# Optimization experiments

Hardware: AMD Instinct MI355X
Metric: run time of the kernel (lower is better)

Reference implementation:

```python
import jax, jax.numpy as jnp
import numpy as np

N = 50000
E = 400000
IN_DIM = 128
OUT_DIM = 512
NUM_MASK = 15000


def _init_linear(key, din, dout):
    s = 1.0 / np.sqrt(din)
    return jax.random.uniform(key, (din, dout), jnp.float32, -s, s)


def setup_inputs() -> dict:
    key = jax.random.key(0)
    ks = jax.random.split(key, 20)
    attr = jax.random.normal(ks[0], (N, IN_DIM), jnp.float32)
    src = jax.random.randint(ks[1], (E,), 0, N, jnp.int32)
    dst = jax.random.randint(ks[2], (E,), 0, N, jnp.int32)
    mask_nodes = jax.random.randint(ks[3], (NUM_MASK,), 0, N, jnp.int32)
    mask_token = jnp.zeros((1, IN_DIM), jnp.float32)
    dims = [(IN_DIM, OUT_DIM), (OUT_DIM, OUT_DIM), (OUT_DIM, OUT_DIM), (OUT_DIM, IN_DIM)]
    params = {}
    for i, (din, dout) in enumerate(dims, start=1):
        params[f"w_self{i}"] = _init_linear(ks[3 * i + 1], din, dout)
        params[f"w_neigh{i}"] = _init_linear(ks[3 * i + 2], din, dout)
        params[f"b{i}"] = jnp.zeros((dout,), jnp.float32)
    return dict(attr=attr, mask_token=mask_token, src=src, dst=dst, mask_nodes=mask_nodes, **params)


def sage_conv(h, src, dst, w_self, w_neigh, b):
    # mean aggregation over in-neighbors (DGL SAGEConv, aggregator_type='mean')
    msg = h[src]                                              # [E, d]
    agg = jax.ops.segment_sum(msg, dst, num_segments=N)       # [N, d]
    deg = jax.ops.segment_sum(jnp.ones((E,), h.dtype), dst, num_segments=N)
    h_neigh = agg / jnp.maximum(deg, 1.0)[:, None]
    return h @ w_self + h_neigh @ w_neigh + b


def reference(attr, mask_token, src, dst, mask_nodes,
              w_self1, w_neigh1, b1, w_self2, w_neigh2, b2,
              w_self3, w_neigh3, b3, w_self4, w_neigh4, b4):
    # mask node features with the mask token
    h = attr.at[mask_nodes].set(mask_token[0])
    h = jax.nn.relu(sage_conv(h, src, dst, w_self1, w_neigh1, b1))
    h = sage_conv(h, src, dst, w_self2, w_neigh2, b2)          # encoded
    h = jax.nn.relu(sage_conv(h, src, dst, w_self3, w_neigh3, b3))
    decoded = sage_conv(h, src, dst, w_self4, w_neigh4, b4)
    x_orig = attr[mask_nodes]
    x_rec = decoded[mask_nodes]
    return jnp.mean((x_rec - x_orig) ** 2)
```

## Files before the change

kernel.cpp:

```cpp
#include <hip/hip_runtime.h>
#include <cstdint>
#include <cstddef>

#define IN_DIM 128
#define HID    512

typedef unsigned int   uint32;
typedef unsigned short u16;
typedef __attribute__((ext_vector_type(8))) short bf16x8;
typedef __attribute__((ext_vector_type(4))) float f32x4;

static inline int imin_h(int a, int b) { return a < b ? a : b; }

__device__ __forceinline__ float bfu2f(uint32 u) { return __uint_as_float(u << 16); }
__device__ __forceinline__ u16 f2bf(float f) {
  uint32 x = __float_as_uint(f);
  x += 0x7fffu + ((x >> 16) & 1u);
  return (u16)(x >> 16);
}
__device__ __forceinline__ uint32 pack2(float a, float b) {
  return (uint32)f2bf(a) | ((uint32)f2bf(b) << 16);
}

#define GLOBAL_AS(p) ((const __attribute__((address_space(1))) void*)(p))
#define LDS_AS(p)    ((__attribute__((address_space(3))) void*)(p))

__global__ void k_zero2(int* __restrict__ a, int na, int* __restrict__ b, int nb) {
  const int total = na + nb;
  for (int i = blockIdx.x * blockDim.x + threadIdx.x; i < total; i += gridDim.x * blockDim.x) {
    if (i < na) a[i] = 0;
    else        b[i - na] = 0;
  }
}

__global__ void k_hist(const int* __restrict__ dst, int* __restrict__ deg, int E) {
  for (int e = blockIdx.x * blockDim.x + threadIdx.x; e < E; e += gridDim.x * blockDim.x)
    atomicAdd(&deg[dst[e]], 1);
}

__global__ __launch_bounds__(256)
void k_scan1(const int* __restrict__ deg, int* __restrict__ bsum, int n) {
  __shared__ int sm[256];
  const int base = blockIdx.x * 2048 + threadIdx.x * 8;
  int s = 0;
  if (base + 8 <= n) {
    const uint4 a = *reinterpret_cast<const uint4*>(deg + base);
    const uint4 b = *reinterpret_cast<const uint4*>(deg + base + 4);
    s = (int)(a.x + a.y + a.z + a.w + b.x + b.y + b.z + b.w);
  } else {
    for (int i = 0; i < 8; ++i) if (base + i < n) s += deg[base + i];
  }
  sm[threadIdx.x] = s;
  __syncthreads();
  for (int off = 128; off > 0; off >>= 1) {
    if (threadIdx.x < off) sm[threadIdx.x] += sm[threadIdx.x + off];
    __syncthreads();
  }
  if (threadIdx.x == 0) bsum[blockIdx.x] = sm[0];
}

__global__ __launch_bounds__(256)
void k_scan2(int* __restrict__ bsum, int nb, int* __restrict__ rowptr, int n) {
  __shared__ int sm[256];
  const int v = (threadIdx.x < nb) ? bsum[threadIdx.x] : 0;
  sm[threadIdx.x] = v;
  __syncthreads();
  for (int off = 1; off < 256; off <<= 1) {
    const int t = (threadIdx.x >= off) ? sm[threadIdx.x - off] : 0;
    __syncthreads();
    sm[threadIdx.x] += t;
    __syncthreads();
  }
  if (threadIdx.x < nb) bsum[threadIdx.x] = sm[threadIdx.x] - v;
  if (threadIdx.x == nb - 1) rowptr[n] = sm[threadIdx.x];
}

__global__ __launch_bounds__(256)
void k_scan3(const int* __restrict__ deg, const int* __restrict__ bsum,
             int* __restrict__ rowptr, int* __restrict__ cursor, int n) {
  __shared__ int sm[256];
  const int base = blockIdx.x * 2048 + threadIdx.x * 8;
  int v[8];
  int s = 0;
#pragma unroll
  for (int i = 0; i < 8; ++i) {
    v[i] = (base + i < n) ? deg[base + i] : 0;
    s += v[i];
  }
  sm[threadIdx.x] = s;
  __syncthreads();
  for (int off = 1; off < 256; off <<= 1) {
    const int t = (threadIdx.x >= off) ? sm[threadIdx.x - off] : 0;
    __syncthreads();
    sm[threadIdx.x] += t;
    __syncthreads();
  }
  int run = bsum[blockIdx.x] + sm[threadIdx.x] - s;
#pragma unroll
  for (int i = 0; i < 8; ++i) {
    if (base + i < n) { rowptr[base + i] = run; cursor[base + i] = run; }
    run += v[i];
  }
}

__global__ void k_fill(const int* __restrict__ src, const int* __restrict__ dst,
                       int* __restrict__ cursor, int* __restrict__ col, int E) {
  for (int e = blockIdx.x * blockDim.x + threadIdx.x; e < E; e += gridDim.x * blockDim.x) {
    const int p = atomicAdd(&cursor[dst[e]], 1);
    col[p] = src[e];
  }
}

__global__ void k_cvt(const float4* __restrict__ in, uint2* __restrict__ out, int n4) {
  for (int i = blockIdx.x * blockDim.x + threadIdx.x; i < n4; i += gridDim.x * blockDim.x) {
    const float4 v = in[i];
    out[i] = make_uint2(pack2(v.x, v.y), pack2(v.z, v.w));
  }
}

__global__ void k_mask(const float4* __restrict__ token, const int* __restrict__ mask,
                       uint2* __restrict__ h0, int NM) {
  const int total = NM * (IN_DIM / 4);
  for (int i = blockIdx.x * blockDim.x + threadIdx.x; i < total; i += gridDim.x * blockDim.x) {
    const int m = i >> 5;
    const int c = i & 31;
    const float4 t = token[c];
    h0[(size_t)mask[m] * (IN_DIM / 4) + c] = make_uint2(pack2(t.x, t.y), pack2(t.z, t.w));
  }
}

struct WtJobs {
  const float* W[8];
  u16* Wt[8];
  int K[8];
  int Nn[8];
  int start[9];
};

__global__ __launch_bounds__(256)
void k_wt_all(WtJobs jobs) {
  const int total = jobs.start[8];
  for (int t = blockIdx.x * blockDim.x + threadIdx.x; t < total; t += gridDim.x * blockDim.x) {
    int s = 0;
#pragma unroll
    for (int i = 0; i < 7; ++i) s += (t >= jobs.start[i + 1]) ? 1 : 0;
    const int loc = t - jobs.start[s];
    const int K = jobs.K[s], Nn = jobs.Nn[s];
    const int n = loc / K, k = loc - n * K;
    const size_t idx = ((size_t)(n >> 4) * (K >> 5) + (k >> 5)) * 512 +
                       ((k >> 3) & 3) * 128 + ((n & 15) << 3) + (k & 7);
    jobs.Wt[s][idx] = f2bf(jobs.W[s][(size_t)k * Nn + n]);
  }
}

template <int D, bool REMAP>
__global__ __launch_bounds__(256)
void k_agg(const u16* __restrict__ h, const int* __restrict__ col,
           const int* __restrict__ rowptr, const int* __restrict__ nodes,
           u16* __restrict__ out, int n) {
  constexpr int V = D / 64;
  const int w = blockIdx.x * (blockDim.x >> 6) + (threadIdx.x >> 6);
  if (w >= n) return;
  const int node = REMAP ? nodes[w] : w;
  const int lane = threadIdx.x & 63;
  const int beg = rowptr[node], end = rowptr[node + 1];
  const size_t loff = (size_t)lane * V;
  float acc[V];
#pragma unroll
  for (int j = 0; j < V; ++j) acc[j] = 0.f;

  if constexpr (V == 8) {
    auto L = [&](int e) {
      return *reinterpret_cast<const uint4*>(h + (size_t)col[e] * D + loff);
    };
    uint4 b0{}, b1{}, b2{}, b3{};
    if (beg + 0 < end) b0 = L(beg + 0);
    if (beg + 1 < end) b1 = L(beg + 1);
    if (beg + 2 < end) b2 = L(beg + 2);
    if (beg + 3 < end) b3 = L(beg + 3);
    for (int e = beg; e < end; e += 4) {
      const uint4 c0 = b0, c1 = b1, c2 = b2, c3 = b3;
      if (e + 4 < end) b0 = L(e + 4);
      if (e + 5 < end) b1 = L(e + 5);
      if (e + 6 < end) b2 = L(e + 6);
      if (e + 7 < end) b3 = L(e + 7);
      acc[0] += bfu2f(c0.x & 0xffffu); acc[1] += bfu2f(c0.x >> 16);
      acc[2] += bfu2f(c0.y & 0xffffu); acc[3] += bfu2f(c0.y >> 16);
      acc[4] += bfu2f(c0.z & 0xffffu); acc[5] += bfu2f(c0.z >> 16);
      acc[6] += bfu2f(c0.w & 0xffffu); acc[7] += bfu2f(c0.w >> 16);
      if (e + 1 < end) {
        acc[0] += bfu2f(c1.x & 0xffffu); acc[1] += bfu2f(c1.x >> 16);
        acc[2] += bfu2f(c1.y & 0xffffu); acc[3] += bfu2f(c1.y >> 16);
        acc[4] += bfu2f(c1.z & 0xffffu); acc[5] += bfu2f(c1.z >> 16);
        acc[6] += bfu2f(c1.w & 0xffffu); acc[7] += bfu2f(c1.w >> 16);
      }
      if (e + 2 < end) {
        acc[0] += bfu2f(c2.x & 0xffffu); acc[1] += bfu2f(c2.x >> 16);
        acc[2] += bfu2f(c2.y & 0xffffu); acc[3] += bfu2f(c2.y >> 16);
        acc[4] += bfu2f(c2.z & 0xffffu); acc[5] += bfu2f(c2.z >> 16);
        acc[6] += bfu2f(c2.w & 0xffffu); acc[7] += bfu2f(c2.w >> 16);
      }
      if (e + 3 < end) {
        acc[0] += bfu2f(c3.x & 0xffffu); acc[1] += bfu2f(c3.x >> 16);
        acc[2] += bfu2f(c3.y & 0xffffu); acc[3] += bfu2f(c3.y >> 16);
        acc[4] += bfu2f(c3.z & 0xffffu); acc[5] += bfu2f(c3.z >> 16);
        acc[6] += bfu2f(c3.w & 0xffffu); acc[7] += bfu2f(c3.w >> 16);
      }
    }
  } else {
    auto L = [&](int e) {
      return *reinterpret_cast<const uint32*>(h + (size_t)col[e] * D + loff);
    };
    uint32 b0 = 0, b1 = 0, b2 = 0, b3 = 0;
    if (beg + 0 < end) b0 = L(beg + 0);
    if (beg + 1 < end) b1 = L(beg + 1);
    if (beg + 2 < end) b2 = L(beg + 2);
    if (beg + 3 < end) b3 = L(beg + 3);
    for (int e = beg; e < end; e += 4) {
      const uint32 c0 = b0, c1 = b1, c2 = b2, c3 = b3;
      if (e + 4 < end) b0 = L(e + 4);
      if (e + 5 < end) b1 = L(e + 5);
      if (e + 6 < end) b2 = L(e + 6);
      if (e + 7 < end) b3 = L(e + 7);
      acc[0] += bfu2f(c0 & 0xffffu); acc[1] += bfu2f(c0 >> 16);
      if (e + 1 < end) { acc[0] += bfu2f(c1 & 0xffffu); acc[1] += bfu2f(c1 >> 16); }
      if (e + 2 < end) { acc[0] += bfu2f(c2 & 0xffffu); acc[1] += bfu2f(c2 >> 16); }
      if (e + 3 < end) { acc[0] += bfu2f(c3 & 0xffffu); acc[1] += bfu2f(c3 >> 16); }
    }
  }

  const float inv = 1.0f / fmaxf((float)(end - beg), 1.0f);
  u16* o = out + (size_t)w * D + loff;
  if constexpr (V == 8) {
    uint4 u;
    u.x = pack2(acc[0] * inv, acc[1] * inv);
    u.y = pack2(acc[2] * inv, acc[3] * inv);
    u.z = pack2(acc[4] * inv, acc[5] * inv);
    u.w = pack2(acc[6] * inv, acc[7] * inv);
    *reinterpret_cast<uint4*>(o) = u;
  } else {
    *reinterpret_cast<uint32*>(o) = pack2(acc[0] * inv, acc[1] * inv);
  }
}

template <int DIN, bool RELU>
__global__ __launch_bounds__(512, 4)
void k_gemm_big(const u16* __restrict__ A1, const u16* __restrict__ A2,
                const u16* __restrict__ Wt1, const u16* __restrict__ Wt2,
                const float* __restrict__ bias, u16* __restrict__ out, int M) {
  constexpr int DOUT = HID;
  __shared__ char lds[73728];
  constexpr int KS = DIN / 32;
  constexpr int S  = 2 * KS;
  const int tid = threadIdx.x;
  const int w = tid >> 6, l = tid & 63;
  const int l15 = l & 15, l4 = l >> 4;
  const int wm = w >> 2, wn = w & 3;

  const int nwg  = gridDim.x * gridDim.y;
  const int orig = blockIdx.x + gridDim.x * blockIdx.y;
  const int q = nwg >> 3, r = nwg & 7;
  const int xcd = orig & 7, seq = orig >> 3;
  const int wg = (xcd < r ? xcd * (q + 1) : r * (q + 1) + (xcd - r) * q) + seq;
  const int mt = wg >> 1, nt = wg & 1;
  const int m0 = mt * 128, n0 = nt * 256;

  f32x4 acc[4][4];
#pragma unroll
  for (int i = 0; i < 4; ++i)
#pragma unroll
    for (int j = 0; j < 4; ++j) acc[i][j] = (f32x4){0.f, 0.f, 0.f, 0.f};

  const int arow = min(m0 + w * 16 + l15, M - 1);
  const int kl = l4 * 8;
  const u16* pA1 = A1 + (size_t)arow * DIN + kl;
  const u16* pA2 = A2 + (size_t)arow * DIN + kl;
  const u16* bb1 = Wt1 + ((size_t)(n0 >> 4) + 2 * w) * KS * 512 + (size_t)l * 8;
  const u16* bb2 = Wt2 + ((size_t)(n0 >> 4) + 2 * w) * KS * 512 + (size_t)l * 8;

  auto stage = [&](int s) {
    const int ph = s / KS;
    const int kf = s - ph * KS;
    char* buf = lds + (s % 3) * 24576;
    const u16* a0 = (ph ? pA2 : pA1) + kf * 32;
    const u16* b0 = (ph ? bb2 : bb1) + kf * 512;
    const u16* b1 = b0 + KS * 512;
    __builtin_amdgcn_global_load_lds(GLOBAL_AS(a0), LDS_AS(buf + w * 1024), 16, 0, 0);
    __builtin_amdgcn_global_load_lds(GLOBAL_AS(b0), LDS_AS(buf + 8192 + (2 * w + 0) * 1024), 16, 0, 0);
    __builtin_amdgcn_global_load_lds(GLOBAL_AS(b1), LDS_AS(buf + 8192 + (2 * w + 1) * 1024), 16, 0, 0);
  };

  stage(0);
  stage(1);

#pragma unroll
  for (int s = 0; s < S; ++s) {
    if (s + 1 < S) asm volatile("s_waitcnt vmcnt(3)" ::: "memory");
    else           asm volatile("s_waitcnt vmcnt(0)" ::: "memory");
    __builtin_amdgcn_s_barrier();
    if (s + 2 < S) stage(s + 2);
    char* buf = lds + (s % 3) * 24576;
    bf16x8 af[4], bfr[4];
#pragma unroll
    for (int i = 0; i < 4; ++i)
      af[i] = *reinterpret_cast<const bf16x8*>(buf + (wm * 4 + i) * 1024 + l * 16);
#pragma unroll
    for (int j = 0; j < 4; ++j)
      bfr[j] = *reinterpret_cast<const bf16x8*>(buf + 8192 + (wn * 4 + j) * 1024 + l * 16);
#pragma unroll
    for (int i = 0; i < 4; ++i)
#pragma unroll
      for (int j = 0; j < 4; ++j)
        acc[i][j] = __builtin_amdgcn_mfma_f32_16x16x32_bf16(af[i], bfr[j], acc[i][j], 0, 0, 0);
    asm volatile("s_waitcnt lgkmcnt(0)" ::: "memory");
  }
  __builtin_amdgcn_s_barrier();

  u16* eb = (u16*)(lds + w * 9216);
  float bv[4];
#pragma unroll
  for (int j = 0; j < 4; ++j) bv[j] = bias[n0 + wn * 64 + j * 16 + l15];
#pragma unroll
  for (int i = 0; i < 4; ++i)
#pragma unroll
    for (int j = 0; j < 4; ++j)
#pragma unroll
      for (int r = 0; r < 4; ++r) {
        const int lr = i * 16 + l4 * 4 + r;
        float t = acc[i][j][r] + bv[j];
        if (RELU) t = fmaxf(t, 0.f);
        eb[lr * 72 + j * 16 + l15] = f2bf(t);
      }
  asm volatile("s_waitcnt lgkmcnt(0)" ::: "memory");
#pragma unroll
  for (int p = 0; p < 8; ++p) {
    const int lr = p * 8 + (l >> 3);
    const int row = m0 + wm * 64 + lr;
    if (row < M) {
      const uint4 v = *reinterpret_cast<const uint4*>(eb + lr * 72 + (l & 7) * 8);
      *reinterpret_cast<uint4*>(out + (size_t)row * DOUT + n0 + wn * 64 + (l & 7) * 8) = v;
    }
  }
}

template <int DIN, int DOUT>
__global__ __launch_bounds__(256, 3)
void k_gemm_loss(const u16* __restrict__ A1, const u16* __restrict__ A2,
                 const u16* __restrict__ Wt1, const u16* __restrict__ Wt2,
                 const float* __restrict__ bias, const float* __restrict__ attr,
                 float* __restrict__ partials, int M, const int* __restrict__ remap) {
  __shared__ char lds[49152];
  constexpr int KS = DIN / 32;
  constexpr int S  = 2 * KS;
  const int tid = threadIdx.x;
  const int w = tid >> 6, l = tid & 63;
  const int l15 = l & 15, l4 = l >> 4;
  const int wm = w >> 1, wn = w & 1;

  const int nwg  = gridDim.x * gridDim.y;
  const int orig = blockIdx.x + gridDim.x * blockIdx.y;
  const int q = nwg >> 3, r = nwg & 7;
  const int xcd = orig & 7, seq = orig >> 3;
  const int wg = (xcd < r ? xcd * (q + 1) : r * (q + 1) + (xcd - r) * q) + seq;
  constexpr int NT = DOUT / 128;
  const int mt = wg / NT, nt = wg - mt * NT;
  const int m0 = mt * 128, n0 = nt * 128;

  f32x4 acc[4][4];
#pragma unroll
  for (int i = 0; i < 4; ++i)
#pragma unroll
    for (int j = 0; j < 4; ++j) acc[i][j] = (f32x4){0.f, 0.f, 0.f, 0.f};

  const int am0 = min(m0 + (2 * w) * 16 + l15, M - 1);
  const int am1 = min(m0 + (2 * w + 1) * 16 + l15, M - 1);
  const int ar0 = remap[am0];
  const int ar1 = remap[am1];
  const int kl = l4 * 8;
  const u16* pA1r0 = A1 + (size_t)ar0 * DIN + kl;
  const u16* pA1r1 = A1 + (size_t)ar1 * DIN + kl;
  const u16* pA2r0 = A2 + (size_t)am0 * DIN + kl;
  const u16* pA2r1 = A2 + (size_t)am1 * DIN + kl;
  const u16* bb1 = Wt1 + ((size_t)(n0 >> 4) + 2 * w) * KS * 512 + (size_t)l * 8;
  const u16* bb2 = Wt2 + ((size_t)(n0 >> 4) + 2 * w) * KS * 512 + (size_t)l * 8;

  auto stage = [&](int s) {
    const int ph = s / KS;
    const int kf = s - ph * KS;
    char* buf = lds + (s % 3) * 16384;
    const u16* a0 = (ph ? pA2r0 : pA1r0) + kf * 32;
    const u16* a1 = (ph ? pA2r1 : pA1r1) + kf * 32;
    const u16* b0 = (ph ? bb2 : bb1) + kf * 512;
    const u16* b1 = b0 + KS * 512;
    __builtin_amdgcn_global_load_lds(GLOBAL_AS(a0), LDS_AS(buf + (2 * w + 0) * 1024), 16, 0, 0);
    __builtin_amdgcn_global_load_lds(GLOBAL_AS(a1), LDS_AS(buf + (2 * w + 1) * 1024), 16, 0, 0);
    __builtin_amdgcn_global_load_lds(GLOBAL_AS(b0), LDS_AS(buf + 8192 + (2 * w + 0) * 1024), 16, 0, 0);
    __builtin_amdgcn_global_load_lds(GLOBAL_AS(b1), LDS_AS(buf + 8192 + (2 * w + 1) * 1024), 16, 0, 0);
  };

  stage(0);
  stage(1);

#pragma unroll
  for (int s = 0; s < S; ++s) {
    if (s + 1 < S) asm volatile("s_waitcnt vmcnt(4)" ::: "memory");
    else           asm volatile("s_waitcnt vmcnt(0)" ::: "memory");
    __builtin_amdgcn_s_barrier();
    if (s + 2 < S) stage(s + 2);
    char* buf = lds + (s % 3) * 16384;
    bf16x8 af[4], bfr[4];
#pragma unroll
    for (int i = 0; i < 4; ++i)
      af[i] = *reinterpret_cast<const bf16x8*>(buf + (wm * 4 + i) * 1024 + l * 16);
#pragma unroll
    for (int j = 0; j < 4; ++j)
      bfr[j] = *reinterpret_cast<const bf16x8*>(buf + 8192 + (wn * 4 + j) * 1024 + l * 16);
#pragma unroll
    for (int i = 0; i < 4; ++i)
#pragma unroll
      for (int j = 0; j < 4; ++j)
        acc[i][j] = __builtin_amdgcn_mfma_f32_16x16x32_bf16(af[i], bfr[j], acc[i][j], 0, 0, 0);
    asm volatile("s_waitcnt lgkmcnt(0)" ::: "memory");
  }

  float lsum = 0.f;
#pragma unroll
  for (int j = 0; j < 4; ++j) {
    const int c = n0 + wn * 64 + j * 16 + l15;
    const float bv = bias[c];
#pragma unroll
    for (int i = 0; i < 4; ++i) {
      const int rowb = m0 + wm * 64 + i * 16 + l4 * 4;
#pragma unroll
      for (int r2 = 0; r2 < 4; ++r2) {
        const int row = rowb + r2;
        if (row < M) {
          const float t = bfu2f((uint32)f2bf(acc[i][j][r2] + bv));
          const float d = t - attr[(size_t)remap[row] * IN_DIM + c];
          lsum += d * d;
        }
      }
    }
  }
  __syncthreads();
  float* sm = (float*)lds;
  sm[tid] = lsum;
  __syncthreads();
  for (int off2 = 128; off2 > 0; off2 >>= 1) {
    if (tid < off2) sm[tid] += sm[tid + off2];
    __syncthreads();
  }
  if (tid == 0) atomicAdd(&partials[0], sm[0]);
}

__global__ void k_final(const float* __restrict__ partials, float* __restrict__ out, float inv) {
  out[0] = partials[0] * inv;
}

extern "C" void kernel_launch(void* const* d_in, const int* in_sizes, int n_in,
                              void* d_out, int out_size, void* d_ws, size_t ws_size,
                              hipStream_t stream) {
  const float* attr  = (const float*)d_in[0];
  const float* token = (const float*)d_in[1];
  const int*   src   = (const int*)d_in[2];
  const int*   dst   = (const int*)d_in[3];
  const int*   mask  = (const int*)d_in[4];
  const float* Wself[4]  = {(const float*)d_in[5], (const float*)d_in[8],
                            (const float*)d_in[11], (const float*)d_in[14]};
  const float* Wneigh[4] = {(const float*)d_in[6], (const float*)d_in[9],
                            (const float*)d_in[12], (const float*)d_in[15]};
  const float* Bias[4]   = {(const float*)d_in[7], (const float*)d_in[10],
                            (const float*)d_in[13], (const float*)d_in[16]};
  const int N  = in_sizes[0] / IN_DIM;
  const int E  = in_sizes[2];
  const int NM = in_sizes[4];

  size_t off = 0;
  auto take = [&](size_t bytes) -> void* {
    void* p = (char*)d_ws + off;
    off += (bytes + 255) & ~(size_t)255;
    return p;
  };
  u16* HA = (u16*)take((size_t)N * HID * sizeof(u16));
  u16* HB = (u16*)take((size_t)N * HID * sizeof(u16));
  const int dims_in[4]  = {IN_DIM, HID, HID, HID};
  const int dims_out[4] = {HID, HID, HID, IN_DIM};
  u16* WtS[4]; u16* WtN[4];
  for (int i = 0; i < 4; ++i) {
    WtS[i] = (u16*)take((size_t)dims_in[i] * dims_out[i] * sizeof(u16));
    WtN[i] = (u16*)take((size_t)dims_in[i] * dims_out[i] * sizeof(u16));
  }
  int* deg    = (int*)take((size_t)N * sizeof(int));
  int* rowptr = (int*)take((size_t)(N + 1) * sizeof(int));
  int* cursor = (int*)take((size_t)N * sizeof(int));
  int* col    = (int*)take((size_t)E * sizeof(int));
  int* bsum   = (int*)take(256 * sizeof(int));
  float* partials = (float*)take(512 * sizeof(float));

  size_t rem = (ws_size > off + 4096) ? (ws_size - off - 4096) : 0;
  const int cap = (int)(rem / ((size_t)HID * sizeof(u16)));
  const int want = (N + 255) & ~255;
  int chunk = (cap >= want) ? want : (cap & ~255);
  if (chunk < 2048) chunk = 2048;
  u16* CH = (u16*)take((size_t)chunk * HID * sizeof(u16));

  k_zero2<<<imin_h((N + 512 + 255) / 256, 1024), 256, 0, stream>>>(deg, N, (int*)partials, 512);
  const int eb = imin_h((E + 255) / 256, 4096);
  k_hist<<<eb, 256, 0, stream>>>(dst, deg, E);
  const int nb = (N + 2047) / 2048;
  k_scan1<<<nb, 256, 0, stream>>>(deg, bsum, N);
  k_scan2<<<1, 256, 0, stream>>>(bsum, nb, rowptr, N);
  k_scan3<<<nb, 256, 0, stream>>>(deg, bsum, rowptr, cursor, N);
  k_fill<<<eb, 256, 0, stream>>>(src, dst, cursor, col, E);

  WtJobs jobs;
  int acc0 = 0;
  for (int i = 0; i < 4; ++i) {
    jobs.W[2 * i] = Wself[i];  jobs.Wt[2 * i] = WtS[i];
    jobs.K[2 * i] = dims_in[i]; jobs.Nn[2 * i] = dims_out[i];
    jobs.start[2 * i] = acc0;   acc0 += dims_in[i] * dims_out[i];
    jobs.W[2 * i + 1] = Wneigh[i]; jobs.Wt[2 * i + 1] = WtN[i];
    jobs.K[2 * i + 1] = dims_in[i]; jobs.Nn[2 * i + 1] = dims_out[i];
    jobs.start[2 * i + 1] = acc0;  acc0 += dims_in[i] * dims_out[i];
  }
  jobs.start[8] = acc0;
  k_wt_all<<<imin_h((acc0 + 255) / 256, 2048), 256, 0, stream>>>(jobs);

  const int n4 = N * (IN_DIM / 4);
  k_cvt<<<imin_h((n4 + 255) / 256, 2048), 256, 0, stream>>>((const float4*)attr, (uint2*)HA, n4);
  k_mask<<<imin_h((NM * (IN_DIM / 4) + 255) / 256, 2048), 256, 0, stream>>>(
      (const float4*)token, mask, (uint2*)HA, NM);

  auto run_layer = [&](const u16* hin, u16* hout, int din, int layer, bool relu) {
    for (int c0 = 0; c0 < N; c0 += chunk) {
      const int mc = imin_h(chunk, N - c0);
      const int ab = (mc + 3) / 4;
      if (din == IN_DIM)
        k_agg<IN_DIM, false><<<ab, 256, 0, stream>>>(hin, col, rowptr + c0, nullptr, CH, mc);
      else
        k_agg<HID, false><<<ab, 256, 0, stream>>>(hin, col, rowptr + c0, nullptr, CH, mc);
      const u16* a1 = hin + (size_t)c0 * din;
      u16* o = hout + (size_t)c0 * HID;
      const int mb = (mc + 127) / 128;
      if (din == IN_DIM && relu)
        k_gemm_big<IN_DIM, true><<<dim3(2, mb), 512, 0, stream>>>(
            a1, CH, WtS[layer], WtN[layer], Bias[layer], o, mc);
      else if (relu)
        k_gemm_big<HID, true><<<dim3(2, mb), 512, 0, stream>>>(
            a1, CH, WtS[layer], WtN[layer], Bias[layer], o, mc);
      else
        k_gemm_big<HID, false><<<dim3(2, mb), 512, 0, stream>>>(
            a1, CH, WtS[layer], WtN[layer], Bias[layer], o, mc);
    }
  };

  run_layer(HA, HB, IN_DIM, 0, true);
  run_layer(HB, HA, HID,    1, false);
  run_layer(HA, HB, HID,    2, true);

  k_agg<HID, true><<<(NM + 3) / 4, 256, 0, stream>>>(HB, col, rowptr, mask, CH, NM);
  k_gemm_loss<HID, IN_DIM><<<dim3(1, (NM + 127) / 128), 256, 0, stream>>>(
      HB, CH, WtS[3], WtN[3], Bias[3], attr, partials, NM, mask);

  k_final<<<1, 1, 0, stream>>>(partials, (float*)d_out, 1.0f / ((float)NM * IN_DIM));
}
```

Baseline: 437.1 us.

## Enlarge per-wave GEMM tile to 4 waves and fuse preprocessing kernels

Restructures the main GEMM from 8 waves with 4x4 MFMA tiles each to 4 waves with 4x8 tiles each, improving register-level reuse of A fragments and halving the wave count per block. Each wave now issues six LDS-bound global loads per stage, and the wait counts and epilogue staging are adjusted to match. Separately, the degree histogram, feature conversion and weight transpose are merged into one kernel, and the CSR fill and mask writes into another, to cut launch overhead. The larger accumulator raises VGPR pressure and lowers occupancy, which could reduce latency hiding.

```diff
diff --git a/kernel.cpp b/kernel.cpp
--- a/kernel.cpp
+++ b/kernel.cpp
@@ -33,9 +33,40 @@
   }
 }
 
-__global__ void k_hist(const int* __restrict__ dst, int* __restrict__ deg, int E) {
-  for (int e = blockIdx.x * blockDim.x + threadIdx.x; e < E; e += gridDim.x * blockDim.x)
-    atomicAdd(&deg[dst[e]], 1);
+struct WtJobs {
+  const float* W[8];
+  u16* Wt[8];
+  int K[8];
+  int Nn[8];
+  int start[9];
+};
+
+__global__ __launch_bounds__(256)
+void k_prep1(const int* __restrict__ dst, int* __restrict__ deg, int E,
+             const float4* __restrict__ attr4, uint2* __restrict__ h0, int n4,
+             WtJobs jobs) {
+  const int wtot = jobs.start[8];
+  const int total = E + n4 + wtot;
+  for (int i = blockIdx.x * blockDim.x + threadIdx.x; i < total; i += gridDim.x * blockDim.x) {
+    if (i < E) {
+      atomicAdd(&deg[dst[i]], 1);
+    } else if (i < E + n4) {
+      const int t = i - E;
+      const float4 v = attr4[t];
+      h0[t] = make_uint2(pack2(v.x, v.y), pack2(v.z, v.w));
+    } else {
+      const int t = i - E - n4;
+      int s = 0;
+#pragma unroll
+      for (int j = 0; j < 7; ++j) s += (t >= jobs.start[j + 1]) ? 1 : 0;
+      const int loc = t - jobs.start[s];
+      const int K = jobs.K[s], Nn = jobs.Nn[s];
+      const int n = loc / K, k = loc - n * K;
+      const size_t idx = ((size_t)(n >> 4) * (K >> 5) + (k >> 5)) * 512 +
+                         ((k >> 3) & 3) * 128 + ((n & 15) << 3) + (k & 7);
+      jobs.Wt[s][idx] = f2bf(jobs.W[s][(size_t)k * Nn + n]);
+    }
+  }
 }
 
 __global__ __launch_bounds__(256)
@@ -103,53 +134,23 @@
   }
 }
 
-__global__ void k_fill(const int* __restrict__ src, const int* __restrict__ dst,
-                       int* __restrict__ cursor, int* __restrict__ col, int E) {
-  for (int e = blockIdx.x * blockDim.x + threadIdx.x; e < E; e += gridDim.x * blockDim.x) {
-    const int p = atomicAdd(&cursor[dst[e]], 1);
-    col[p] = src[e];
-  }
-}
-
-__global__ void k_cvt(const float4* __restrict__ in, uint2* __restrict__ out, int n4) {
-  for (int i = blockIdx.x * blockDim.x + threadIdx.x; i < n4; i += gridDim.x * blockDim.x) {
-    const float4 v = in[i];
-    out[i] = make_uint2(pack2(v.x, v.y), pack2(v.z, v.w));
-  }
-}
-
-__global__ void k_mask(const float4* __restrict__ token, const int* __restrict__ mask,
-                       uint2* __restrict__ h0, int NM) {
-  const int total = NM * (IN_DIM / 4);
+__global__ void k_fillmask(const int* __restrict__ src, const int* __restrict__ dst,
+                           int* __restrict__ cursor, int* __restrict__ col, int E,
+                           const float4* __restrict__ token, const int* __restrict__ mask,
+                           uint2* __restrict__ h0, int NM) {
+  const int mtot = NM * (IN_DIM / 4);
+  const int total = E + mtot;
   for (int i = blockIdx.x * blockDim.x + threadIdx.x; i < total; i += gridDim.x * blockDim.x) {
-    const int m = i >> 5;
-    const int c = i & 31;
-    const float4 t = token[c];
-    h0[(size_t)mask[m] * (IN_DIM / 4) + c] = make_uint2(pack2(t.x, t.y), pack2(t.z, t.w));
-  }
-}
-
-struct WtJobs {
-  const float* W[8];
-  u16* Wt[8];
-  int K[8];
-  int Nn[8];
-  int start[9];
-};
-
-__global__ __launch_bounds__(256)
-void k_wt_all(WtJobs jobs) {
-  const int total = jobs.start[8];
-  for (int t = blockIdx.x * blockDim.x + threadIdx.x; t < total; t += gridDim.x * blockDim.x) {
-    int s = 0;
-#pragma unroll
-    for (int i = 0; i < 7; ++i) s += (t >= jobs.start[i + 1]) ? 1 : 0;
-    const int loc = t - jobs.start[s];
-    const int K = jobs.K[s], Nn = jobs.Nn[s];
-    const int n = loc / K, k = loc - n * K;
-    const size_t idx = ((size_t)(n >> 4) * (K >> 5) + (k >> 5)) * 512 +
-                       ((k >> 3) & 3) * 128 + ((n & 15) << 3) + (k & 7);
-    jobs.Wt[s][idx] = f2bf(jobs.W[s][(size_t)k * Nn + n]);
+    if (i < E) {
+      const int p = atomicAdd(&cursor[dst[i]], 1);
+      col[p] = src[i];
+    } else {
+      const int t = i - E;
+      const int m = t >> 5;
+      const int c = t & 31;
+      const float4 tv = token[c];
+      h0[(size_t)mask[m] * (IN_DIM / 4) + c] = make_uint2(pack2(tv.x, tv.y), pack2(tv.z, tv.w));
+    }
   }
 }
 
@@ -244,7 +245,7 @@
 }
 
 template <int DIN, bool RELU>
-__global__ __launch_bounds__(512, 4)
+__global__ __launch_bounds__(256, 2)
 void k_gemm_big(const u16* __restrict__ A1, const u16* __restrict__ A2,
                 const u16* __restrict__ Wt1, const u16* __restrict__ Wt2,
                 const float* __restrict__ bias, u16* __restrict__ out, int M) {
@@ -255,7 +256,7 @@
   const int tid = threadIdx.x;
   const int w = tid >> 6, l = tid & 63;
   const int l15 = l & 15, l4 = l >> 4;
-  const int wm = w >> 2, wn = w & 3;
+  const int wm = w >> 1, wn = w & 1;
 
   const int nwg  = gridDim.x * gridDim.y;
   const int orig = blockIdx.x + gridDim.x * blockIdx.y;
@@ -265,29 +266,35 @@
   const int mt = wg >> 1, nt = wg & 1;
   const int m0 = mt * 128, n0 = nt * 256;
 
-  f32x4 acc[4][4];
+  f32x4 acc[4][8];
 #pragma unroll
   for (int i = 0; i < 4; ++i)
 #pragma unroll
-    for (int j = 0; j < 4; ++j) acc[i][j] = (f32x4){0.f, 0.f, 0.f, 0.f};
-
-  const int arow = min(m0 + w * 16 + l15, M - 1);
+    for (int j = 0; j < 8; ++j) acc[i][j] = (f32x4){0.f, 0.f, 0.f, 0.f};
+
+  const int ar0 = min(m0 + (2 * w + 0) * 16 + l15, M - 1);
+  const int ar1 = min(m0 + (2 * w + 1) * 16 + l15, M - 1);
   const int kl = l4 * 8;
-  const u16* pA1 = A1 + (size_t)arow * DIN + kl;
-  const u16* pA2 = A2 + (size_t)arow * DIN + kl;
-  const u16* bb1 = Wt1 + ((size_t)(n0 >> 4) + 2 * w) * KS * 512 + (size_t)l * 8;
-  const u16* bb2 = Wt2 + ((size_t)(n0 >> 4) + 2 * w) * KS * 512 + (size_t)l * 8;
+  const u16* pA1r0 = A1 + (size_t)ar0 * DIN + kl;
+  const u16* pA1r1 = A1 + (size_t)ar1 * DIN + kl;
+  const u16* pA2r0 = A2 + (size_t)ar0 * DIN + kl;
+  const u16* pA2r1 = A2 + (size_t)ar1 * DIN + kl;
+  const u16* bb1 = Wt1 + ((size_t)(n0 >> 4) + 4 * w) * KS * 512 + (size_t)l * 8;
+  const u16* bb2 = Wt2 + ((size_t)(n0 >> 4) + 4 * w) * KS * 512 + (size_t)l * 8;
 
   auto stage = [&](int s) {
     const int ph = s / KS;
     const int kf = s - ph * KS;
     char* buf = lds + (s % 3) * 24576;
-    const u16* a0 = (ph ? pA2 : pA1) + kf * 32;
-    const u16* b0 = (ph ? bb2 : bb1) + kf * 512;
-    const u16* b1 = b0 + KS * 512;
-    __builtin_amdgcn_global_load_lds(GLOBAL_AS(a0), LDS_AS(buf + w * 1024), 16, 0, 0);
-    __builtin_amdgcn_global_load_lds(GLOBAL_AS(b0), LDS_AS(buf + 8192 + (2 * w + 0) * 1024), 16, 0, 0);
-    __builtin_amdgcn_global_load_lds(GLOBAL_AS(b1), LDS_AS(buf + 8192 + (2 * w + 1) * 1024), 16, 0, 0);
+    const u16* a0 = (ph ? pA2r0 : pA1r0) + kf * 32;
+    const u16* a1 = (ph ? pA2r1 : pA1r1) + kf * 32;
+    const u16* b  = (ph ? bb2 : bb1) + kf * 512;
+    __builtin_amdgcn_global_load_lds(GLOBAL_AS(a0), LDS_AS(buf + (2 * w + 0) * 1024), 16, 0, 0);
+    __builtin_amdgcn_global_load_lds(GLOBAL_AS(a1), LDS_AS(buf + (2 * w + 1) * 1024), 16, 0, 0);
+#pragma unroll
+    for (int t = 0; t < 4; ++t)
+      __builtin_amdgcn_global_load_lds(GLOBAL_AS(b + (size_t)t * KS * 512),
+                                       LDS_AS(buf + 8192 + (4 * w + t) * 1024), 16, 0, 0);
   };
 
   stage(0);
@@ -295,50 +302,50 @@
 
 #pragma unroll
   for (int s = 0; s < S; ++s) {
-    if (s + 1 < S) asm volatile("s_waitcnt vmcnt(3)" ::: "memory");
+    if (s + 1 < S) asm volatile("s_waitcnt vmcnt(6)" ::: "memory");
     else           asm volatile("s_waitcnt vmcnt(0)" ::: "memory");
     __builtin_amdgcn_s_barrier();
     if (s + 2 < S) stage(s + 2);
     char* buf = lds + (s % 3) * 24576;
-    bf16x8 af[4], bfr[4];
+    bf16x8 af[4], bfr[8];
 #pragma unroll
     for (int i = 0; i < 4; ++i)
       af[i] = *reinterpret_cast<const bf16x8*>(buf + (wm * 4 + i) * 1024 + l * 16);
 #pragma unroll
-    for (int j = 0; j < 4; ++j)
-      bfr[j] = *reinterpret_cast<const bf16x8*>(buf + 8192 + (wn * 4 + j) * 1024 + l * 16);
+    for (int j = 0; j < 8; ++j)
+      bfr[j] = *reinterpret_cast<const bf16x8*>(buf + 8192 + (wn * 8 + j) * 1024 + l * 16);
 #pragma unroll
     for (int i = 0; i < 4; ++i)
 #pragma unroll
-      for (int j = 0; j < 4; ++j)
+      for (int j = 0; j < 8; ++j)
         acc[i][j] = __builtin_amdgcn_mfma_f32_16x16x32_bf16(af[i], bfr[j], acc[i][j], 0, 0, 0);
     asm volatile("s_waitcnt lgkmcnt(0)" ::: "memory");
   }
   __builtin_amdgcn_s_barrier();
 
-  u16* eb = (u16*)(lds + w * 9216);
-  float bv[4];
-#pragma unroll
-  for (int j = 0; j < 4; ++j) bv[j] = bias[n0 + wn * 64 + j * 16 + l15];
+  u16* eb = (u16*)(lds + w * 17408);
+  float bv[8];
+#pragma unroll
+  for (int j = 0; j < 8; ++j) bv[j] = bias[n0 + wn * 128 + j * 16 + l15];
 #pragma unroll
   for (int i = 0; i < 4; ++i)
 #pragma unroll
-    for (int j = 0; j < 4; ++j)
+    for (int j = 0; j < 8; ++j)
 #pragma unroll
       for (int r = 0; r < 4; ++r) {
         const int lr = i * 16 + l4 * 4 + r;
         float t = acc[i][j][r] + bv[j];
         if (RELU) t = fmaxf(t, 0.f);
-        eb[lr * 72 + j * 16 + l15] = f2bf(t);
+        eb[lr * 136 + j * 16 + l15] = f2bf(t);
       }
   asm volatile("s_waitcnt lgkmcnt(0)" ::: "memory");
 #pragma unroll
-  for (int p = 0; p < 8; ++p) {
-    const int lr = p * 8 + (l >> 3);
+  for (int p = 0; p < 16; ++p) {
+    const int lr = p * 4 + (l >> 4);
     const int row = m0 + wm * 64 + lr;
     if (row < M) {
-      const uint4 v = *reinterpret_cast<const uint4*>(eb + lr * 72 + (l & 7) * 8);
-      *reinterpret_cast<uint4*>(out + (size_t)row * DOUT + n0 + wn * 64 + (l & 7) * 8) = v;
+      const uint4 v = *reinterpret_cast<const uint4*>(eb + lr * 136 + l15 * 8);
+      *reinterpret_cast<uint4*>(out + (size_t)row * DOUT + n0 + wn * 128 + l15 * 8) = v;
     }
   }
 }
@@ -505,13 +512,6 @@
   u16* CH = (u16*)take((size_t)chunk * HID * sizeof(u16));
 
   k_zero2<<<imin_h((N + 512 + 255) / 256, 1024), 256, 0, stream>>>(deg, N, (int*)partials, 512);
-  const int eb = imin_h((E + 255) / 256, 4096);
-  k_hist<<<eb, 256, 0, stream>>>(dst, deg, E);
-  const int nb = (N + 2047) / 2048;
-  k_scan1<<<nb, 256, 0, stream>>>(deg, bsum, N);
-  k_scan2<<<1, 256, 0, stream>>>(bsum, nb, rowptr, N);
-  k_scan3<<<nb, 256, 0, stream>>>(deg, bsum, rowptr, cursor, N);
-  k_fill<<<eb, 256, 0, stream>>>(src, dst, cursor, col, E);
 
   WtJobs jobs;
   int acc0 = 0;
@@ -524,12 +524,19 @@
     jobs.start[2 * i + 1] = acc0;  acc0 += dims_in[i] * dims_out[i];
   }
   jobs.start[8] = acc0;
-  k_wt_all<<<imin_h((acc0 + 255) / 256, 2048), 256, 0, stream>>>(jobs);
-
   const int n4 = N * (IN_DIM / 4);
-  k_cvt<<<imin_h((n4 + 255) / 256, 2048), 256, 0, stream>>>((const float4*)attr, (uint2*)HA, n4);
-  k_mask<<<imin_h((NM * (IN_DIM / 4) + 255) / 256, 2048), 256, 0, stream>>>(
-      (const float4*)token, mask, (uint2*)HA, NM);
+  const int p1 = E + n4 + acc0;
+  k_prep1<<<imin_h((p1 + 255) / 256, 4096), 256, 0, stream>>>(
+      dst, deg, E, (const float4*)attr, (uint2*)HA, n4, jobs);
+
+  const int nb = (N + 2047) / 2048;
+  k_scan1<<<nb, 256, 0, stream>>>(deg, bsum, N);
+  k_scan2<<<1, 256, 0, stream>>>(bsum, nb, rowptr, N);
+  k_scan3<<<nb, 256, 0, stream>>>(deg, bsum, rowptr, cursor, N);
+
+  const int p2 = E + NM * (IN_DIM / 4);
+  k_fillmask<<<imin_h((p2 + 255) / 256, 4096), 256, 0, stream>>>(
+      src, dst, cursor, col, E, (const float4*)token, mask, (uint2*)HA, NM);
 
   auto run_layer = [&](const u16* hin, u16* hout, int din, int layer, bool relu) {
     for (int c0 = 0; c0 < N; c0 += chunk) {
@@ -543,13 +550,13 @@
       u16* o = hout + (size_t)c0 * HID;
       const int mb = (mc + 127) / 128;
       if (din == IN_DIM && relu)
-        k_gemm_big<IN_DIM, true><<<dim3(2, mb), 512, 0, stream>>>(
+        k_gemm_big<IN_DIM, true><<<dim3(2, mb), 256, 0, stream>>>(
             a1, CH, WtS[layer], WtN[layer], Bias[layer], o, mc);
       else if (relu)
-        k_gemm_big<HID, true><<<dim3(2, mb), 512, 0, stream>>>(
+        k_gemm_big<HID, true><<<dim3(2, mb), 256, 0, stream>>>(
             a1, CH, WtS[layer], WtN[layer], Bias[layer], o, mc);
       else
-        k_gemm_big<HID, false><<<dim3(2, mb), 512, 0, stream>>>(
+        k_gemm_big<HID, false><<<dim3(2, mb), 256, 0, stream>>>(
             a1, CH, WtS[layer], WtN[layer], Bias[layer], o, mc);
     }
   };
```

Measured after the change: 433.7 us. Within noise of the previous version (-0.8%).
